# Kernel optimization log

Hardware: AMD Instinct MI355X
Metric: run time of the kernel (lower is better)

Reference implementation:

```python
import jax, jax.numpy as jnp
import numpy as np

D = 1280
RANK = 4

def _lora(x, down, up):
    # x: [..., in]; down: [r, in]; up: [out, r]
    return (x @ down.T) @ up.T

def setup_inputs() -> dict:
    key = jax.random.key(0)
    ks = jax.random.split(key, 15)
    B, S = 4, 2048
    inp = {
        'hidden_states': jax.random.normal(ks[0], (B, S, D), jnp.float32),
        'Wq': jax.random.normal(ks[1], (D, D), jnp.float32) * (D ** -0.5),
        'Wk': jax.random.normal(ks[2], (D, D), jnp.float32) * (D ** -0.5),
        'Wv': jax.random.normal(ks[3], (D, D), jnp.float32) * (D ** -0.5),
        'Wo': jax.random.normal(ks[4], (D, D), jnp.float32) * (D ** -0.5),
        'bo': jax.random.normal(ks[5], (D,), jnp.float32) * 0.02,
        'q_down': jax.random.normal(ks[6], (RANK, D), jnp.float32) / RANK,
        'q_up': jax.random.normal(ks[7], (D, RANK), jnp.float32) * 0.02,
        'k_down': jax.random.normal(ks[8], (RANK, D), jnp.float32) / RANK,
        'k_up': jax.random.normal(ks[9], (D, RANK), jnp.float32) * 0.02,
        'v_down': jax.random.normal(ks[10], (RANK, D), jnp.float32) / RANK,
        'v_up': jax.random.normal(ks[11], (D, RANK), jnp.float32) * 0.02,
        'o_down': jax.random.normal(ks[12], (RANK, D), jnp.float32) / RANK,
        'o_up': jax.random.normal(ks[13], (D, RANK), jnp.float32) * 0.02,
        'num_heads': 8,
    }
    return inp

def reference(hidden_states, Wq, Wk, Wv, Wo, bo, q_down, q_up, k_down, k_up,
              v_down, v_up, o_down, o_up, num_heads):
    B, S, Dm = hidden_states.shape
    H = num_heads
    hd = Dm // H
    scale = hd ** -0.5
    x = hidden_states
    # base projections + rank-4 LoRA deltas (self-attention: enc == x)
    q = x @ Wq.T + _lora(x, q_down, q_up)
    k = x @ Wk.T + _lora(x, k_down, k_up)
    v = x @ Wv.T + _lora(x, v_down, v_up)
    q = q.reshape(B, S, H, hd)
    k = k.reshape(B, S, H, hd)
    v = v.reshape(B, S, H, hd)
    # explicit bmm -> softmax -> bmm attention (no mask, no norm_cross)
    scores = jnp.einsum('bqhd,bkhd->bhqk', q, k) * scale  # [B,H,S,S]
    probs = jax.nn.softmax(scores, axis=-1)
    ctx = jnp.einsum('bhqk,bkhd->bqhd', probs, v).reshape(B, S, Dm)
    # output projection (with bias) + LoRA on output; dropout is identity at eval
    out = ctx @ Wo.T + bo + _lora(ctx, o_down, o_up)
    return out
```

## Files before the change

kernel.cpp:

```cpp
#include <hip/hip_runtime.h>
#include <cstdint>

typedef _Float16 f16;
typedef f16 f16x8 __attribute__((ext_vector_type(8)));
typedef f16 f16x4 __attribute__((ext_vector_type(4)));
typedef f16 f16x2 __attribute__((ext_vector_type(2)));
typedef float f32x4 __attribute__((ext_vector_type(4)));
typedef uint32_t u32x4 __attribute__((ext_vector_type(4)));

#define D_MODEL 1280
#define SEQ 2048
#define BATCH 4
#define HEADS 8
#define HDIM 160
#define MTOT (BATCH*SEQ)
#define NQKV (3*D_MODEL)

__device__ __forceinline__ void gload_lds16(const f16* g, f16* l) {
  __builtin_amdgcn_global_load_lds(
      (const __attribute__((address_space(1))) unsigned int*)g,
      (__attribute__((address_space(3))) unsigned int*)l,
      16, 0, 0);
}

#define BARX() { asm volatile("" ::: "memory"); __builtin_amdgcn_s_barrier(); asm volatile("" ::: "memory"); }
#define VMW(N) { asm volatile("s_waitcnt vmcnt(" #N ")" ::: "memory"); }


__global__ void convert_f32_to_f16(const float* __restrict__ in, f16* __restrict__ out, int n4) {
  int i = blockIdx.x * 256 + threadIdx.x;
  if (i < n4) {
    float4 v = ((const float4*)in)[i];
    f16x4 o = { (f16)v.x, (f16)v.y, (f16)v.z, (f16)v.w };
    ((f16x4*)out)[i] = o;
  }
}

__global__ void build_weff(const float* __restrict__ W, const float* __restrict__ up,
                           const float* __restrict__ down, f16* __restrict__ out) {
  int idx = blockIdx.x * 256 + threadIdx.x;
  int o  = idx / (D_MODEL / 4);
  int i0 = (idx % (D_MODEL / 4)) * 4;
  float4 w = *(const float4*)&W[(size_t)o * D_MODEL + i0];
  float u0 = up[o*4+0], u1 = up[o*4+1], u2 = up[o*4+2], u3 = up[o*4+3];
  float vals[4] = { w.x, w.y, w.z, w.w };
  f16x4 r;
#pragma unroll
  for (int j = 0; j < 4; ++j) {
    int i = i0 + j;
    float acc = vals[j] + u0*down[i] + u1*down[D_MODEL + i]
                        + u2*down[2*D_MODEL + i] + u3*down[3*D_MODEL + i];
    r[j] = (f16)acc;
  }
  *(f16x4*)&out[(size_t)o * D_MODEL + i0] = r;
}

__global__ void transpose_v(const f16* __restrict__ qkv, f16* __restrict__ Vt) {
  __shared__ f16 t[32][36];
  int s0 = blockIdx.x * 32;
  int d0 = blockIdx.y * 32;
  int bh = blockIdx.z;
  int b = bh >> 3, h = bh & 7;
  int tid = threadIdx.x;
  {
    int i = tid >> 3, j4 = (tid & 7) * 4;
    *(f16x4*)&t[i][j4] =
        *(const f16x4*)&qkv[(size_t)(b*SEQ + s0 + i) * NQKV + 2*D_MODEL + h*HDIM + d0 + j4];
  }
  __syncthreads();
  {
    int dd = tid >> 3, s4 = (tid & 7) * 4;
    f16x4 v;
#pragma unroll
    for (int k = 0; k < 4; ++k) {
      int s = s4 + k;
      int sj = (((s>>2) ^ (s>>3)) & 1) ? (s ^ 12) : s;
      v[k] = t[sj][dd];
    }
    *(f16x4*)&Vt[(size_t)(bh*HDIM + d0 + dd) * SEQ + s0 + s4] = v;
  }
}

template<int OUTF32>
__global__ __launch_bounds__(512) void gemm256(const f16* __restrict__ A,
                                               const f16* __restrict__ Bw,
                                               void* __restrict__ Cp, int ldc,
                                               const float* __restrict__ bias) {
  const int K = D_MODEL, NT = D_MODEL/64;
  __shared__ alignas(16) f16 lds[7 * 8192];
  f16* LB = lds + 3*8192;
  int tid = threadIdx.x;
  int wv = tid >> 6, l = tid & 63;
  int wm = wv >> 2, wn = wv & 3;
  int lr = l & 15, lg = l >> 4;

  int flat = blockIdx.y * gridDim.x + blockIdx.x;
  int bnn = gridDim.x;
  int xcd = flat & 7, idx = flat >> 3;
  int bm = xcd * 4 + idx / bnn;
  int bn = idx % bnn;

  int row0 = tid >> 3;
  int csw  = ((tid & 7) ^ (row0 & 7)) * 8;
  const f16* Asrc[2]; const f16* Bsrc[2];
#pragma unroll
  for (int h = 0; h < 2; ++h) {
    Asrc[h] = A  + (size_t)(bm*256 + h*128 + row0) * K + csw;
    Bsrc[h] = Bw + (size_t)(bn*256 + h*128 + row0) * K + csw;
  }
  int ldsoff = wv * 512;

  int xsl0 = ((lg)     ^ (lr & 7)) * 8;
  int xsl1 = ((4 + lg) ^ (lr & 7)) * 8;

  f32x4 acc[8][4] = {};

#define STAGE_A(h, slot, kt) { const f16* s_ = Asrc[h] + (kt)*64; f16* d_ = lds + (slot)*8192 + ldsoff; \
    gload_lds16(s_, d_); gload_lds16(s_ + (size_t)64*K, d_ + 4096); }
#define STAGE_B(h, slot, kt) { const f16* s_ = Bsrc[h] + (kt)*64; f16* d_ = LB + (slot)*8192 + ldsoff; \
    gload_lds16(s_, d_); gload_lds16(s_ + (size_t)64*K, d_ + 4096); }

  STAGE_A(0, 0, 0); STAGE_A(1, 1, 0);
  STAGE_B(0, 0, 0); STAGE_B(1, 1, 0);
  STAGE_B(0, 2, 1);
  VMW(2); BARX();

  for (int t = 0; t < NT; ++t) {
    int sA0 = (2*t) % 3, sA1 = (2*t+1) % 3, sA2 = (2*t+2) % 3;
    int sB0 = (2*t) & 3, sB1 = (2*t+1) & 3, sB3 = (2*t+3) & 3;
    int tc1 = (t+1 < NT) ? t+1 : NT-1;
    int tc2 = (t+2 < NT) ? t+2 : NT-1;

#define PHASE(ah, bh, sA, sB, STG, VMOPT) { \
    f16x8 af[4][2], bf[2][2]; \
    _Pragma("unroll") \
    for (int j = 0; j < 4; ++j) { \
      int base = (sA)*8192 + (wm*64 + j*16 + lr)*64; \
      af[j][0] = *(const f16x8*)&lds[base + xsl0]; \
      af[j][1] = *(const f16x8*)&lds[base + xsl1]; \
    } \
    _Pragma("unroll") \
    for (int i = 0; i < 2; ++i) { \
      int base = (sB)*8192 + (wn*32 + i*16 + lr)*64; \
      bf[i][0] = *(const f16x8*)&LB[base + xsl0]; \
      bf[i][1] = *(const f16x8*)&LB[base + xsl1]; \
    } \
    STG; \
    BARX(); \
    __builtin_amdgcn_s_setprio(1); \
    _Pragma("unroll") \
    for (int j = 0; j < 4; ++j) \
      _Pragma("unroll") \
      for (int i = 0; i < 2; ++i) { \
        acc[(ah)*4+j][(bh)*2+i] = __builtin_amdgcn_mfma_f32_16x16x32_f16(af[j][0], bf[i][0], acc[(ah)*4+j][(bh)*2+i], 0, 0, 0); \
        acc[(ah)*4+j][(bh)*2+i] = __builtin_amdgcn_mfma_f32_16x16x32_f16(af[j][1], bf[i][1], acc[(ah)*4+j][(bh)*2+i], 0, 0, 0); \
      } \
    __builtin_amdgcn_s_setprio(0); \
    VMOPT; \
    BARX(); }

    PHASE(0, 0, sA0, sB0, STAGE_B(1, sB3, tc1), VMW(2))
    PHASE(1, 0, sA1, sB0, STAGE_A(0, sA2, tc1), )
    PHASE(0, 1, sA0, sB1, STAGE_B(0, sB0, tc2), )
    PHASE(1, 1, sA1, sB1, STAGE_A(1, sA0, tc1), VMW(4))
#undef PHASE
  }

#pragma unroll
  for (int mf = 0; mf < 8; ++mf) {
    int r0 = bm*256 + (mf>>2)*128 + wm*64 + (mf&3)*16 + lg*4;
#pragma unroll
    for (int nf = 0; nf < 4; ++nf) {
      int c = bn*256 + (nf>>1)*128 + wn*32 + (nf&1)*16 + lr;
      if constexpr (OUTF32) {
        float bb = bias[c];
#pragma unroll
        for (int rg = 0; rg < 4; ++rg)
          ((float*)Cp)[(size_t)(r0 + rg) * ldc + c] = acc[mf][nf][rg] + bb;
      } else {
#pragma unroll
        for (int rg = 0; rg < 4; ++rg)
          ((f16*)Cp)[(size_t)(r0 + rg) * ldc + c] = (f16)acc[mf][nf][rg];
      }
    }
  }
#undef STAGE_A
#undef STAGE_B
}

__global__ __launch_bounds__(256, 2) void attn(const f16* __restrict__ qkv,
                                               const f16* __restrict__ Vt,
                                               f16* __restrict__ ctx) {
  __shared__ alignas(16) f16 Kl[64 * 168];
  __shared__ alignas(16) f16 Vl[160 * 64];
  int tid = threadIdx.x;
  int wv = tid >> 6, l = tid & 63;
  int lr = l & 15, lg = l >> 4;
  int flat = blockIdx.y * 16 + blockIdx.x;
  int xcd = flat & 7, idx = flat >> 3;
  int bh = xcd * 4 + (idx >> 4);
  int qt = idx & 15;
  int b = bh >> 3, h = bh & 7;
  size_t qrow[2];
#pragma unroll
  for (int qg = 0; qg < 2; ++qg)
    qrow[qg] = (size_t)(b*SEQ + qt*128 + wv*32 + qg*16 + lr);

  const f16 qscale = (f16)0.114055069f;
  f16x8 qf[2][5];
#pragma unroll
  for (int qg = 0; qg < 2; ++qg)
#pragma unroll
    for (int dk = 0; dk < 5; ++dk) {
      f16x8 t = *(const f16x8*)&qkv[qrow[qg] * NQKV + h*HDIM + dk*32 + lg*8];
#pragma unroll
      for (int j = 0; j < 8; ++j) t[j] = t[j] * qscale;
      qf[qg][dk] = t;
    }

  const char* Kg0 = (const char*)qkv + (size_t)(b*SEQ)*NQKV*2 + (size_t)D_MODEL*2 + (size_t)h*HDIM*2;
  char* KlB = (char*)Kl;
  uint32_t koff[6];
  f16* kld[6];
#pragma unroll
  for (int it = 0; it < 6; ++it) {
    int p = (it < 5) ? it*256 + tid : 1280 + (tid & 63);
    koff[it] = (uint32_t)(p/21) * (NQKV*2) + (uint32_t)(p%21) * 16;
    kld[it] = (f16*)(KlB + ((it < 5) ? (it*256 + wv*64)*16 : 1280*16));
  }

  const char* Vg0 = (const char*)Vt + (size_t)bh*HDIM*SEQ*2;
  char* VlB = (char*)Vl;
  uint32_t voff[5];
  f16* vld[5];
#pragma unroll
  for (int it = 0; it < 5; ++it) {
    int c = it*256 + tid;
    int row = c >> 3, sp = c & 7;
    voff[it] = (uint32_t)row * (SEQ*2) + (uint32_t)((sp ^ (row & 7)) * 16);
    vld[it] = (f16*)(VlB + (it*256 + wv*64)*16);
  }
  uint32_t vro[2];
#pragma unroll
  for (int ks = 0; ks < 2; ++ks)
    vro[ks] = (uint32_t)lr*128 + (uint32_t)((((ks*4+lg) ^ (lr & 7)) * 16));

  f32x4 oacc[10][2] = {};
  float m[2] = {-1e30f, -1e30f}, lsum[2] = {0.f, 0.f};

  for (int kt = 0; kt < 32; ++kt) {
    const char* Ksrc = Kg0 + (size_t)kt * (64*NQKV*2);
    const char* Vsrc = Vg0 + (size_t)kt * 128;
#pragma unroll
    for (int it = 0; it < 5; ++it) {
      gload_lds16((const f16*)(Ksrc + koff[it]), kld[it]);
      gload_lds16((const f16*)(Vsrc + voff[it]), vld[it]);
    }
    if (wv == 0)
      gload_lds16((const f16*)(Ksrc + koff[5]), kld[5]);
    __syncthreads();

    f32x4 sc[4][2] = {};
    __builtin_amdgcn_s_setprio(1);
#pragma unroll
    for (int kb = 0; kb < 4; ++kb)
#pragma unroll
      for (int dk = 0; dk < 5; ++dk) {
        f16x8 a = *(const f16x8*)&Kl[(kb*16 + lr)*168 + dk*32 + lg*8];
        sc[kb][0] = __builtin_amdgcn_mfma_f32_16x16x32_f16(a, qf[0][dk], sc[kb][0], 0, 0, 0);
        sc[kb][1] = __builtin_amdgcn_mfma_f32_16x16x32_f16(a, qf[1][dk], sc[kb][1], 0, 0, 0);
      }
    __builtin_amdgcn_s_setprio(0);

    float smax[2];
#pragma unroll
    for (int qg = 0; qg < 2; ++qg) {
      float sm = -1e30f;
#pragma unroll
      for (int kb = 0; kb < 4; ++kb)
#pragma unroll
        for (int rg = 0; rg < 4; ++rg) sm = fmaxf(sm, sc[kb][qg][rg]);
      sm = fmaxf(sm, __shfl_xor(sm, 16));
      sm = fmaxf(sm, __shfl_xor(sm, 32));
      smax[qg] = sm;
    }
    if (!__all(fmaxf(smax[0] - m[0], smax[1] - m[1]) <= 11.54f)) {
#pragma unroll
      for (int qg = 0; qg < 2; ++qg) {
        float mn = fmaxf(m[qg], smax[qg]);
        float alpha = exp2f(m[qg] - mn);
#pragma unroll
        for (int df = 0; df < 10; ++df)
#pragma unroll
          for (int rg = 0; rg < 4; ++rg) oacc[df][qg][rg] *= alpha;
        lsum[qg] *= alpha;
        m[qg] = mn;
      }
    }

    f16x8 pb[2][2];
#pragma unroll
    for (int qg = 0; qg < 2; ++qg) {
      float ps[16];
      float psum = 0.f;
#pragma unroll
      for (int kb = 0; kb < 4; ++kb)
#pragma unroll
        for (int rg = 0; rg < 4; ++rg) {
          float p = exp2f(sc[kb][qg][rg] - m[qg]);
          ps[kb*4 + rg] = p;
          psum += p;
        }
      psum += __shfl_xor(psum, 16);
      psum += __shfl_xor(psum, 32);
      lsum[qg] += psum;

      uint32_t w0, w1, w2, w3, w4, w5, w6, w7;
      asm("v_cvt_pkrtz_f16_f32 %0, %1, %2" : "=v"(w0) : "v"(ps[0]),  "v"(ps[1]));
      asm("v_cvt_pkrtz_f16_f32 %0, %1, %2" : "=v"(w1) : "v"(ps[2]),  "v"(ps[3]));
      asm("v_cvt_pkrtz_f16_f32 %0, %1, %2" : "=v"(w2) : "v"(ps[4]),  "v"(ps[5]));
      asm("v_cvt_pkrtz_f16_f32 %0, %1, %2" : "=v"(w3) : "v"(ps[6]),  "v"(ps[7]));
      asm("v_cvt_pkrtz_f16_f32 %0, %1, %2" : "=v"(w4) : "v"(ps[8]),  "v"(ps[9]));
      asm("v_cvt_pkrtz_f16_f32 %0, %1, %2" : "=v"(w5) : "v"(ps[10]), "v"(ps[11]));
      asm("v_cvt_pkrtz_f16_f32 %0, %1, %2" : "=v"(w6) : "v"(ps[12]), "v"(ps[13]));
      asm("v_cvt_pkrtz_f16_f32 %0, %1, %2" : "=v"(w7) : "v"(ps[14]), "v"(ps[15]));
      asm("v_permlane32_swap_b32 %0, %1" : "+v"(w0), "+v"(w2));
      asm("v_permlane32_swap_b32 %0, %1" : "+v"(w1), "+v"(w3));
      asm("v_permlane32_swap_b32 %0, %1" : "+v"(w4), "+v"(w6));
      asm("v_permlane32_swap_b32 %0, %1" : "+v"(w5), "+v"(w7));
      u32x4 c0 = { w0, w1, w2, w3 };
      u32x4 c1 = { w4, w5, w6, w7 };
      pb[qg][0] = __builtin_bit_cast(f16x8, c0);
      pb[qg][1] = __builtin_bit_cast(f16x8, c1);
    }

    __builtin_amdgcn_s_setprio(1);
#pragma unroll
    for (int df = 0; df < 10; ++df)
#pragma unroll
      for (int ks = 0; ks < 2; ++ks) {
        f16x8 a = *(const f16x8*)(VlB + vro[ks] + df*2048);
        oacc[df][0] = __builtin_amdgcn_mfma_f32_16x16x32_f16(a, pb[0][ks], oacc[df][0], 0, 0, 0);
        oacc[df][1] = __builtin_amdgcn_mfma_f32_16x16x32_f16(a, pb[1][ks], oacc[df][1], 0, 0, 0);
      }
    __builtin_amdgcn_s_setprio(0);
    __syncthreads();
  }

#pragma unroll
  for (int qg = 0; qg < 2; ++qg) {
    float inv = 1.f / lsum[qg];
#pragma unroll
    for (int df = 0; df < 10; ++df)
#pragma unroll
      for (int pr = 0; pr < 2; ++pr) {
        f16x2 pv = { (f16)(oacc[df][qg][pr*2+0] * inv), (f16)(oacc[df][qg][pr*2+1] * inv) };
        *(f16x2*)&ctx[qrow[qg] * D_MODEL + h*HDIM + df*16 + lg*4 + pr*2] = pv;
      }
  }
}


extern "C" void kernel_launch(void* const* d_in, const int* in_sizes, int n_in,
                              void* d_out, int out_size, void* d_ws, size_t ws_size,
                              hipStream_t stream) {
  const float* x   = (const float*)d_in[0];
  const float* Wq  = (const float*)d_in[1];
  const float* Wk  = (const float*)d_in[2];
  const float* Wv  = (const float*)d_in[3];
  const float* Wo  = (const float*)d_in[4];
  const float* bo  = (const float*)d_in[5];
  const float* q_down = (const float*)d_in[6];
  const float* q_up   = (const float*)d_in[7];
  const float* k_down = (const float*)d_in[8];
  const float* k_up   = (const float*)d_in[9];
  const float* v_down = (const float*)d_in[10];
  const float* v_up   = (const float*)d_in[11];
  const float* o_down = (const float*)d_in[12];
  const float* o_up   = (const float*)d_in[13];
  float* out = (float*)d_out;

  char* ws = (char*)d_ws;
  f16* xh    = (f16*)ws;
  f16* Wqkv  = (f16*)(ws + 20971520);
  f16* WoE   = (f16*)(ws + 20971520 + 9830400);
  f16* qkv   = (f16*)(ws + 20971520 + 9830400 + 3276800);
  f16* Vt    = (f16*)(ws + 20971520 + 9830400 + 3276800 + 62914560);
  f16* ctx   = xh;

  convert_f32_to_f16<<<(MTOT*D_MODEL/4 + 255)/256, 256, 0, stream>>>(x, xh, MTOT*D_MODEL/4);
  build_weff<<<D_MODEL*D_MODEL/4/256, 256, 0, stream>>>(Wq, q_up, q_down, Wqkv);
  build_weff<<<D_MODEL*D_MODEL/4/256, 256, 0, stream>>>(Wk, k_up, k_down, Wqkv + (size_t)D_MODEL*D_MODEL);
  build_weff<<<D_MODEL*D_MODEL/4/256, 256, 0, stream>>>(Wv, v_up, v_down, Wqkv + (size_t)2*D_MODEL*D_MODEL);
  build_weff<<<D_MODEL*D_MODEL/4/256, 256, 0, stream>>>(Wo, o_up, o_down, WoE);

  gemm256<0><<<dim3(NQKV/256, MTOT/256), 512, 0, stream>>>(xh, Wqkv, qkv, NQKV, nullptr);
  transpose_v<<<dim3(SEQ/32, HDIM/32, BATCH*HEADS), 256, 0, stream>>>(qkv, Vt);
  attn<<<dim3(SEQ/128, BATCH*HEADS), 256, 0, stream>>>(qkv, Vt, ctx);
  gemm256<1><<<dim3(D_MODEL/256, MTOT/256), 512, 0, stream>>>(ctx, WoE, out, D_MODEL, bo);
  (void)in_sizes; (void)n_in; (void)out_size; (void)ws_size;
}
```

Measured before the change: 282.5 us.

## Double-buffer K tiles and prefetch K/V asynchronously in attention loop

Makes the K shared-memory tile double-buffered and restructures the attention loop into a software pipeline. The K load for tile kt+2 is issued right after the QK MFMAs, and the V load for kt+1 right after the PV MFMAs, with explicit vmcnt waits and barriers in place of a full sync per tile. The goal is to hide global-to-LDS load latency behind softmax and MFMA work. It doubles K LDS usage, which may affect occupancy at two blocks per CU. It also relies on VMW/BARX macros defined elsewhere and on exact vmcnt counting being correct.

```diff
diff --git a/kernel.cpp b/kernel.cpp
--- a/kernel.cpp
+++ b/kernel.cpp
@@ -191,7 +191,7 @@
 __global__ __launch_bounds__(256, 2) void attn(const f16* __restrict__ qkv,
                                                const f16* __restrict__ Vt,
                                                f16* __restrict__ ctx) {
-  __shared__ alignas(16) f16 Kl[64 * 168];
+  __shared__ alignas(16) f16 Kl[2][64 * 168];
   __shared__ alignas(16) f16 Vl[160 * 64];
   int tid = threadIdx.x;
   int wv = tid >> 6, l = tid & 63;
@@ -217,16 +217,15 @@
       for (int j = 0; j < 8; ++j) t[j] = t[j] * qscale;
       qf[qg][dk] = t;
     }
+  VMW(0);
 
   const char* Kg0 = (const char*)qkv + (size_t)(b*SEQ)*NQKV*2 + (size_t)D_MODEL*2 + (size_t)h*HDIM*2;
-  char* KlB = (char*)Kl;
-  uint32_t koff[6];
-  f16* kld[6];
+  uint32_t koff[6], kldo[6];
 #pragma unroll
   for (int it = 0; it < 6; ++it) {
     int p = (it < 5) ? it*256 + tid : 1280 + (tid & 63);
     koff[it] = (uint32_t)(p/21) * (NQKV*2) + (uint32_t)(p%21) * 16;
-    kld[it] = (f16*)(KlB + ((it < 5) ? (it*256 + wv*64)*16 : 1280*16));
+    kldo[it] = (it < 5) ? (uint32_t)(it*256 + wv*64)*16 : 1280*16;
   }
 
   const char* Vg0 = (const char*)Vt + (size_t)bh*HDIM*SEQ*2;
@@ -248,104 +247,117 @@
   f32x4 oacc[10][2] = {};
   float m[2] = {-1e30f, -1e30f}, lsum[2] = {0.f, 0.f};
 
-  for (int kt = 0; kt < 32; ++kt) {
-    const char* Ksrc = Kg0 + (size_t)kt * (64*NQKV*2);
-    const char* Vsrc = Vg0 + (size_t)kt * 128;
-#pragma unroll
-    for (int it = 0; it < 5; ++it) {
-      gload_lds16((const f16*)(Ksrc + koff[it]), kld[it]);
-      gload_lds16((const f16*)(Vsrc + voff[it]), vld[it]);
-    }
-    if (wv == 0)
-      gload_lds16((const f16*)(Ksrc + koff[5]), kld[5]);
-    __syncthreads();
-
-    f32x4 sc[4][2] = {};
-    __builtin_amdgcn_s_setprio(1);
-#pragma unroll
-    for (int kb = 0; kb < 4; ++kb)
-#pragma unroll
-      for (int dk = 0; dk < 5; ++dk) {
-        f16x8 a = *(const f16x8*)&Kl[(kb*16 + lr)*168 + dk*32 + lg*8];
-        sc[kb][0] = __builtin_amdgcn_mfma_f32_16x16x32_f16(a, qf[0][dk], sc[kb][0], 0, 0, 0);
-        sc[kb][1] = __builtin_amdgcn_mfma_f32_16x16x32_f16(a, qf[1][dk], sc[kb][1], 0, 0, 0);
-      }
-    __builtin_amdgcn_s_setprio(0);
-
-    float smax[2];
-#pragma unroll
-    for (int qg = 0; qg < 2; ++qg) {
-      float sm = -1e30f;
-#pragma unroll
-      for (int kb = 0; kb < 4; ++kb)
-#pragma unroll
-        for (int rg = 0; rg < 4; ++rg) sm = fmaxf(sm, sc[kb][qg][rg]);
-      sm = fmaxf(sm, __shfl_xor(sm, 16));
-      sm = fmaxf(sm, __shfl_xor(sm, 32));
-      smax[qg] = sm;
-    }
-    if (!__all(fmaxf(smax[0] - m[0], smax[1] - m[1]) <= 11.54f)) {
-#pragma unroll
-      for (int qg = 0; qg < 2; ++qg) {
-        float mn = fmaxf(m[qg], smax[qg]);
-        float alpha = exp2f(m[qg] - mn);
-#pragma unroll
-        for (int df = 0; df < 10; ++df)
-#pragma unroll
-          for (int rg = 0; rg < 4; ++rg) oacc[df][qg][rg] *= alpha;
-        lsum[qg] *= alpha;
-        m[qg] = mn;
-      }
-    }
-
-    f16x8 pb[2][2];
-#pragma unroll
-    for (int qg = 0; qg < 2; ++qg) {
-      float ps[16];
-      float psum = 0.f;
-#pragma unroll
-      for (int kb = 0; kb < 4; ++kb)
-#pragma unroll
-        for (int rg = 0; rg < 4; ++rg) {
-          float p = exp2f(sc[kb][qg][rg] - m[qg]);
-          ps[kb*4 + rg] = p;
-          psum += p;
-        }
-      psum += __shfl_xor(psum, 16);
-      psum += __shfl_xor(psum, 32);
-      lsum[qg] += psum;
-
-      uint32_t w0, w1, w2, w3, w4, w5, w6, w7;
-      asm("v_cvt_pkrtz_f16_f32 %0, %1, %2" : "=v"(w0) : "v"(ps[0]),  "v"(ps[1]));
-      asm("v_cvt_pkrtz_f16_f32 %0, %1, %2" : "=v"(w1) : "v"(ps[2]),  "v"(ps[3]));
-      asm("v_cvt_pkrtz_f16_f32 %0, %1, %2" : "=v"(w2) : "v"(ps[4]),  "v"(ps[5]));
-      asm("v_cvt_pkrtz_f16_f32 %0, %1, %2" : "=v"(w3) : "v"(ps[6]),  "v"(ps[7]));
-      asm("v_cvt_pkrtz_f16_f32 %0, %1, %2" : "=v"(w4) : "v"(ps[8]),  "v"(ps[9]));
-      asm("v_cvt_pkrtz_f16_f32 %0, %1, %2" : "=v"(w5) : "v"(ps[10]), "v"(ps[11]));
-      asm("v_cvt_pkrtz_f16_f32 %0, %1, %2" : "=v"(w6) : "v"(ps[12]), "v"(ps[13]));
-      asm("v_cvt_pkrtz_f16_f32 %0, %1, %2" : "=v"(w7) : "v"(ps[14]), "v"(ps[15]));
-      asm("v_permlane32_swap_b32 %0, %1" : "+v"(w0), "+v"(w2));
-      asm("v_permlane32_swap_b32 %0, %1" : "+v"(w1), "+v"(w3));
-      asm("v_permlane32_swap_b32 %0, %1" : "+v"(w4), "+v"(w6));
-      asm("v_permlane32_swap_b32 %0, %1" : "+v"(w5), "+v"(w7));
-      u32x4 c0 = { w0, w1, w2, w3 };
-      u32x4 c1 = { w4, w5, w6, w7 };
-      pb[qg][0] = __builtin_bit_cast(f16x8, c0);
-      pb[qg][1] = __builtin_bit_cast(f16x8, c1);
-    }
-
-    __builtin_amdgcn_s_setprio(1);
-#pragma unroll
-    for (int df = 0; df < 10; ++df)
-#pragma unroll
-      for (int ks = 0; ks < 2; ++ks) {
-        f16x8 a = *(const f16x8*)(VlB + vro[ks] + df*2048);
-        oacc[df][0] = __builtin_amdgcn_mfma_f32_16x16x32_f16(a, pb[0][ks], oacc[df][0], 0, 0, 0);
-        oacc[df][1] = __builtin_amdgcn_mfma_f32_16x16x32_f16(a, pb[1][ks], oacc[df][1], 0, 0, 0);
-      }
-    __builtin_amdgcn_s_setprio(0);
-    __syncthreads();
-  }
+#define STAGE_K(kt, CUR) { const char* Ks_ = Kg0 + (size_t)(kt)*(64*NQKV*2); \
+    _Pragma("unroll") \
+    for (int it = 0; it < 6; ++it) \
+      gload_lds16((const f16*)(Ks_ + koff[it]), (f16*)((char*)Kl[CUR] + kldo[it])); }
+#define STAGE_V(kt) { const char* Vs_ = Vg0 + (size_t)(kt)*128; \
+    _Pragma("unroll") \
+    for (int it = 0; it < 5; ++it) \
+      gload_lds16((const f16*)(Vs_ + voff[it]), vld[it]); }
+
+  STAGE_K(0, 0);
+  STAGE_V(0);
+  STAGE_K(1, 1);
+  VMW(11); BARX();
+
+#define ITER(ktc, CUR) { \
+    f32x4 sc[4][2] = {}; \
+    __builtin_amdgcn_s_setprio(1); \
+    _Pragma("unroll") \
+    for (int kb = 0; kb < 4; ++kb) \
+      _Pragma("unroll") \
+      for (int dk = 0; dk < 5; ++dk) { \
+        f16x8 a = *(const f16x8*)&Kl[CUR][(kb*16 + lr)*168 + dk*32 + lg*8]; \
+        sc[kb][0] = __builtin_amdgcn_mfma_f32_16x16x32_f16(a, qf[0][dk], sc[kb][0], 0, 0, 0); \
+        sc[kb][1] = __builtin_amdgcn_mfma_f32_16x16x32_f16(a, qf[1][dk], sc[kb][1], 0, 0, 0); \
+      } \
+    __builtin_amdgcn_s_setprio(0); \
+    BARX();   \
+    { int k2_ = (ktc)+2 < 32 ? (ktc)+2 : 31; STAGE_K(k2_, CUR); } \
+    float smax[2]; \
+    _Pragma("unroll") \
+    for (int qg = 0; qg < 2; ++qg) { \
+      float sm = -1e30f; \
+      _Pragma("unroll") \
+      for (int kb = 0; kb < 4; ++kb) \
+        _Pragma("unroll") \
+        for (int rg = 0; rg < 4; ++rg) sm = fmaxf(sm, sc[kb][qg][rg]); \
+      sm = fmaxf(sm, __shfl_xor(sm, 16)); \
+      sm = fmaxf(sm, __shfl_xor(sm, 32)); \
+      smax[qg] = sm; \
+    } \
+    if (!__all(fmaxf(smax[0] - m[0], smax[1] - m[1]) <= 11.54f)) { \
+      _Pragma("unroll") \
+      for (int qg = 0; qg < 2; ++qg) { \
+        float mn = fmaxf(m[qg], smax[qg]); \
+        float alpha = exp2f(m[qg] - mn); \
+        _Pragma("unroll") \
+        for (int df = 0; df < 10; ++df) \
+          _Pragma("unroll") \
+          for (int rg = 0; rg < 4; ++rg) oacc[df][qg][rg] *= alpha; \
+        lsum[qg] *= alpha; \
+        m[qg] = mn; \
+      } \
+    } \
+    f16x8 pb[2][2]; \
+    _Pragma("unroll") \
+    for (int qg = 0; qg < 2; ++qg) { \
+      float ps[16]; \
+      float psum = 0.f; \
+      _Pragma("unroll") \
+      for (int kb = 0; kb < 4; ++kb) \
+        _Pragma("unroll") \
+        for (int rg = 0; rg < 4; ++rg) { \
+          float p = exp2f(sc[kb][qg][rg] - m[qg]); \
+          ps[kb*4 + rg] = p; \
+          psum += p; \
+        } \
+      psum += __shfl_xor(psum, 16); \
+      psum += __shfl_xor(psum, 32); \
+      lsum[qg] += psum; \
+      uint32_t w0, w1, w2, w3, w4, w5, w6, w7; \
+      asm("v_cvt_pkrtz_f16_f32 %0, %1, %2" : "=v"(w0) : "v"(ps[0]),  "v"(ps[1])); \
+      asm("v_cvt_pkrtz_f16_f32 %0, %1, %2" : "=v"(w1) : "v"(ps[2]),  "v"(ps[3])); \
+      asm("v_cvt_pkrtz_f16_f32 %0, %1, %2" : "=v"(w2) : "v"(ps[4]),  "v"(ps[5])); \
+      asm("v_cvt_pkrtz_f16_f32 %0, %1, %2" : "=v"(w3) : "v"(ps[6]),  "v"(ps[7])); \
+      asm("v_cvt_pkrtz_f16_f32 %0, %1, %2" : "=v"(w4) : "v"(ps[8]),  "v"(ps[9])); \
+      asm("v_cvt_pkrtz_f16_f32 %0, %1, %2" : "=v"(w5) : "v"(ps[10]), "v"(ps[11])); \
+      asm("v_cvt_pkrtz_f16_f32 %0, %1, %2" : "=v"(w6) : "v"(ps[12]), "v"(ps[13])); \
+      asm("v_cvt_pkrtz_f16_f32 %0, %1, %2" : "=v"(w7) : "v"(ps[14]), "v"(ps[15])); \
+      asm("v_permlane32_swap_b32 %0, %1" : "+v"(w0), "+v"(w2)); \
+      asm("v_permlane32_swap_b32 %0, %1" : "+v"(w1), "+v"(w3)); \
+      asm("v_permlane32_swap_b32 %0, %1" : "+v"(w4), "+v"(w6)); \
+      asm("v_permlane32_swap_b32 %0, %1" : "+v"(w5), "+v"(w7)); \
+      u32x4 c0 = { w0, w1, w2, w3 }; \
+      u32x4 c1 = { w4, w5, w6, w7 }; \
+      pb[qg][0] = __builtin_bit_cast(f16x8, c0); \
+      pb[qg][1] = __builtin_bit_cast(f16x8, c1); \
+    } \
+    VMW(6); BARX();   \
+    __builtin_amdgcn_s_setprio(1); \
+    _Pragma("unroll") \
+    for (int df = 0; df < 10; ++df) \
+      _Pragma("unroll") \
+      for (int ks = 0; ks < 2; ++ks) { \
+        f16x8 a = *(const f16x8*)(VlB + vro[ks] + df*2048); \
+        oacc[df][0] = __builtin_amdgcn_mfma_f32_16x16x32_f16(a, pb[0][ks], oacc[df][0], 0, 0, 0); \
+        oacc[df][1] = __builtin_amdgcn_mfma_f32_16x16x32_f16(a, pb[1][ks], oacc[df][1], 0, 0, 0); \
+      } \
+    __builtin_amdgcn_s_setprio(0); \
+    BARX();   \
+    { int k1_ = (ktc)+1 < 32 ? (ktc)+1 : 31; STAGE_V(k1_); } \
+  }
+
+  for (int kt = 0; kt < 32; kt += 2) {
+    ITER(kt, 0)
+    ITER(kt + 1, 1)
+  }
+#undef ITER
+#undef STAGE_K
+#undef STAGE_V
+
+  VMW(0);
 
 #pragma unroll
   for (int qg = 0; qg < 2; ++qg) {
```

Measured after the change: 287.7 us. No clear change (+1.9%).
